# Kernel optimization log

Measured on AMD Instinct MI355X. Metric: run time of the kernel, lower is better.

## Reference

```python
import jax, jax.numpy as jnp
import numpy as np

N, E = 100000, 640000
IN_DIM, OUT_DIM, MSG_DIM, TIME_DIM, HEADS = 128, 128, 128, 128, 2
C = OUT_DIM // HEADS  # per-head channels = 64
EDGE_DIM = MSG_DIM + TIME_DIM  # 256


def setup_inputs() -> dict:
    key = jax.random.key(0)
    ks = jax.random.split(key, 16)
    s = 0.05
    return {
        "x": jax.random.normal(ks[0], (N, IN_DIM), jnp.float32),
        "last_update": jax.random.uniform(ks[1], (N,), jnp.float32, 0.0, 100.0),
        "t": jax.random.uniform(ks[2], (E,), jnp.float32, 100.0, 200.0),
        "msg": jax.random.normal(ks[3], (E, MSG_DIM), jnp.float32),
        "time_w": jax.random.normal(ks[4], (TIME_DIM,), jnp.float32) * s,
        "time_b": jax.random.normal(ks[5], (TIME_DIM,), jnp.float32) * s,
        "Wq": jax.random.normal(ks[6], (IN_DIM, HEADS * C), jnp.float32) * s,
        "bq": jnp.zeros((HEADS * C,), jnp.float32),
        "Wk": jax.random.normal(ks[7], (IN_DIM, HEADS * C), jnp.float32) * s,
        "bk": jnp.zeros((HEADS * C,), jnp.float32),
        "Wv": jax.random.normal(ks[8], (IN_DIM, HEADS * C), jnp.float32) * s,
        "bv": jnp.zeros((HEADS * C,), jnp.float32),
        "We": jax.random.normal(ks[9], (EDGE_DIM, HEADS * C), jnp.float32) * s,
        "Wskip": jax.random.normal(ks[10], (IN_DIM, HEADS * C), jnp.float32) * s,
        "bskip": jnp.zeros((HEADS * C,), jnp.float32),
        "edge_index": jax.random.randint(ks[11], (2, E), 0, N, jnp.int64),
    }


def reference(x, last_update, t, msg, time_w, time_b, Wq, bq, Wk, bk, Wv, bv,
              We, Wskip, bskip, edge_index):
    src = edge_index[0]  # source node j per edge
    dst = edge_index[1]  # target node i per edge

    # Time encoding: phi(dt) = cos(w*dt + b)
    rel_t = t - last_update[src]                      # [E]
    rel_t_enc = jnp.cos(rel_t[:, None] * time_w[None, :] + time_b)  # [E, TIME_DIM]
    edge_attr = jnp.concatenate([rel_t_enc, msg], axis=-1)           # [E, EDGE_DIM]

    # Node-level projections (dense GEMMs), then edge gathers
    q_n = x @ Wq + bq   # [N, H*C]
    k_n = x @ Wk + bk
    v_n = x @ Wv + bv
    e_proj = (edge_attr @ We).reshape(E, HEADS, C)    # [E, H, C]

    q = q_n[dst].reshape(E, HEADS, C)
    k = k_n[src].reshape(E, HEADS, C) + e_proj
    v = v_n[src].reshape(E, HEADS, C) + e_proj

    # Per-edge attention logits, scatter-softmax over incoming edges of each dst
    alpha = jnp.sum(q * k, axis=-1) / jnp.sqrt(jnp.float32(C))  # [E, H]
    a_max = jax.ops.segment_max(alpha, dst, num_segments=N)      # [N, H]
    a_max = jnp.where(jnp.isfinite(a_max), a_max, 0.0)
    a_exp = jnp.exp(alpha - a_max[dst])                          # [E, H]
    a_sum = jax.ops.segment_sum(a_exp, dst, num_segments=N)      # [N, H]
    attn = a_exp / (a_sum[dst] + 1e-16)                          # [E, H]

    # Weighted aggregate + skip connection (concat heads)
    out = jax.ops.segment_sum(attn[..., None] * v, dst, num_segments=N)  # [N, H, C]
    out = out.reshape(N, HEADS * C) + (x @ Wskip + bskip)
    return out
```

## Files before the change

kernel.cpp:

```cpp
#include <hip/hip_runtime.h>
#include <hip/hip_bf16.h>

#define NN 100000
#define EE 640000
#define NB_SCAN 98
#define G_E3 2048

typedef short bf16x8 __attribute__((ext_vector_type(8)));
typedef float f32x4 __attribute__((ext_vector_type(4)));

__device__ __forceinline__ ushort f2bf(float f){
  uint u = __float_as_uint(f);
  u += 0x7fffu + ((u >> 16) & 1u);
  return (ushort)(u >> 16);
}
__device__ __forceinline__ float bf2f(ushort s){ return __uint_as_float(((uint)s) << 16); }
__device__ __forceinline__ uint pack2(float a, float b){ return ((uint)f2bf(b) << 16) | (uint)f2bf(a); }
__device__ __forceinline__ uint swz(uint row, uint colB, uint strideB){
  return row * strideB + (colB ^ ((row & 7u) << 4));
}

__global__ void k_prep(const float* __restrict__ Wq, const float* __restrict__ Wk,
                       const float* __restrict__ Wv, const float* __restrict__ Wsk,
                       const float* __restrict__ We,
                       ushort* __restrict__ W4t, ushort* __restrict__ Wet,
                       int* __restrict__ deg){
  int tid = blockIdx.x * 256 + threadIdx.x;
  if (tid < 512 * 128){
    int col = tid >> 7, k = tid & 127;
    const float* W = (col < 128) ? Wq : ((col < 256) ? Wk : ((col < 384) ? Wv : Wsk));
    W4t[tid] = f2bf(W[k * 128 + (col & 127)]);
  }
  if (tid < 128 * 256){
    int col = tid >> 8, k = tid & 255;
    Wet[tid] = f2bf(We[k * 128 + col]);
  }
  if (tid < NN) deg[tid] = 0;
}

__global__ __launch_bounds__(256) void k_node(
    const float* __restrict__ x, const ushort* __restrict__ W4t,
    const float* __restrict__ bq, const float* __restrict__ bk,
    const float* __restrict__ bv, const float* __restrict__ bsk,
    ushort* __restrict__ q_n, ushort* __restrict__ kv,
    float* __restrict__ out){
  __shared__ ushort As[64 * 128];
  __shared__ ushort Bs[128 * 128];
  char* Ab = (char*)As; char* Bb = (char*)Bs;
  int tid = threadIdx.x;
  int n0 = blockIdx.x * 64;
  {
    int row = tid >> 2, part = tid & 3;
    int gr = n0 + row;
    for (int j = 0; j < 4; j++){
      float4 a = make_float4(0.f,0.f,0.f,0.f), b = a;
      if (gr < NN){
        const float4* p = (const float4*)(x + (size_t)gr * 128 + part * 32 + j * 8);
        a = p[0]; b = p[1];
      }
      uint4 w; w.x = pack2(a.x,a.y); w.y = pack2(a.z,a.w); w.z = pack2(b.x,b.y); w.w = pack2(b.z,b.w);
      *(uint4*)(Ab + swz(row, (uint)(part * 64 + j * 16), 256)) = w;
    }
  }
  int wid = tid >> 6, l = tid & 63, lr = l & 15, lg = l >> 4;
  for (int chunk = 0; chunk < 4; ++chunk){
    if (chunk) __syncthreads();
    {
      int row = tid >> 1, half = tid & 1;
      const ushort* src = W4t + (size_t)(chunk * 128 + row) * 128 + half * 64;
      for (int j = 0; j < 8; j++){
        uint4 w = *(const uint4*)(src + j * 8);
        *(uint4*)(Bb + swz(row, (uint)(half * 128 + j * 16), 256)) = w;
      }
    }
    __syncthreads();
    f32x4 acc[8];
    for (int i = 0; i < 8; i++) acc[i] = (f32x4){0.f,0.f,0.f,0.f};
    for (int ks = 0; ks < 4; ++ks){
      bf16x8 a = *(bf16x8*)(Ab + swz(wid * 16 + lr, (uint)(ks * 64 + lg * 16), 256));
      for (int cf = 0; cf < 8; ++cf){
        bf16x8 b = *(bf16x8*)(Bb + swz(cf * 16 + lr, (uint)(ks * 64 + lg * 16), 256));
        acc[cf] = __builtin_amdgcn_mfma_f32_16x16x32_bf16(a, b, acc[cf], 0, 0, 0);
      }
    }
    for (int cf = 0; cf < 8; ++cf){
      for (int i = 0; i < 4; i++){
        int row = wid * 16 + lg * 4 + i;
        int gr = n0 + row;
        if (gr >= NN) continue;
        int col = cf * 16 + lr;
        float v = acc[cf][i];
        if (chunk == 0)      q_n[(size_t)gr * 128 + col] = f2bf(v + bq[col]);
        else if (chunk == 1) kv[(size_t)gr * 256 + ((col >> 1) << 2) + (col & 1)]     = f2bf(v + bk[col]);
        else if (chunk == 2) kv[(size_t)gr * 256 + ((col >> 1) << 2) + 2 + (col & 1)] = f2bf(v + bv[col]);
        else                 out[(size_t)gr * 128 + col] = v + bsk[col];
      }
    }
  }
}

__global__ void k_rel(const float* __restrict__ tt, const float* __restrict__ lu,
                      const int* __restrict__ ei, float* __restrict__ rel){
  int e = blockIdx.x * 256 + threadIdx.x;
  if (e < EE) rel[e] = tt[e] - lu[ei[e]];
}

__global__ __launch_bounds__(256, 2) void k_edge3(
    const float* __restrict__ rel, const float* __restrict__ msg,
    const float* __restrict__ tw, const float* __restrict__ tb,
    const ushort* __restrict__ Wet, ushort* __restrict__ ep){
  int tid = threadIdx.x;
  int wid = tid >> 6, l = tid & 63, lr = l & 15, lg = l >> 4;
  int gw = (int)blockIdx.x * 4 + wid;
  int half = gw & 1;
  bf16x8 Af[4][8];
  const char* WB = (const char*)Wet;
  #pragma unroll
  for (int rt = 0; rt < 4; ++rt)
    #pragma unroll
    for (int ks = 0; ks < 8; ++ks)
      Af[rt][ks] = *(const bf16x8*)(WB + (size_t)(half*64 + rt*16 + lr)*512 + ks*64 + lg*16);

  for (int g = gw >> 1; g < EE/16; g += G_E3 * 2){
    int e0 = g * 16;
    float4 m[8];
    const float* MB = msg + (size_t)(e0 + lr) * 128 + lg * 8;
    #pragma unroll
    for (int ks = 0; ks < 4; ++ks){
      m[2*ks]   = *(const float4*)(MB + ks * 32);
      m[2*ks+1] = *(const float4*)(MB + ks * 32 + 4);
    }
    float relv = rel[e0 + lr];
    bf16x8 B[8];
    #pragma unroll
    for (int ks = 0; ks < 4; ++ks){
      int k0 = ks * 32 + lg * 8;
      float4 wa = *(const float4*)(tw + k0), wb = *(const float4*)(tw + k0 + 4);
      float4 ba = *(const float4*)(tb + k0), bb = *(const float4*)(tb + k0 + 4);
      float c0 = __cosf(fmaf(relv, wa.x, ba.x));
      float c1 = __cosf(fmaf(relv, wa.y, ba.y));
      float c2 = __cosf(fmaf(relv, wa.z, ba.z));
      float c3 = __cosf(fmaf(relv, wa.w, ba.w));
      float c4 = __cosf(fmaf(relv, wb.x, bb.x));
      float c5 = __cosf(fmaf(relv, wb.y, bb.y));
      float c6 = __cosf(fmaf(relv, wb.z, bb.z));
      float c7 = __cosf(fmaf(relv, wb.w, bb.w));
      uint4 w; w.x = pack2(c0,c1); w.y = pack2(c2,c3); w.z = pack2(c4,c5); w.w = pack2(c6,c7);
      B[ks] = *(bf16x8*)&w;
    }
    #pragma unroll
    for (int ks = 0; ks < 4; ++ks){
      float4 a = m[2*ks], b = m[2*ks+1];
      uint4 w; w.x = pack2(a.x,a.y); w.y = pack2(a.z,a.w); w.z = pack2(b.x,b.y); w.w = pack2(b.z,b.w);
      B[4+ks] = *(bf16x8*)&w;
    }
    f32x4 acc[4];
    #pragma unroll
    for (int rt = 0; rt < 4; ++rt) acc[rt] = (f32x4){0.f,0.f,0.f,0.f};
    #pragma unroll
    for (int ks = 0; ks < 8; ++ks)
      #pragma unroll
      for (int rt = 0; rt < 4; ++rt)
        acc[rt] = __builtin_amdgcn_mfma_f32_16x16x32_bf16(Af[rt][ks], B[ks], acc[rt], 0, 0, 0);
    #pragma unroll
    for (int rt = 0; rt < 4; ++rt){
      uint2 w = make_uint2(pack2(acc[rt][0], acc[rt][1]), pack2(acc[rt][2], acc[rt][3]));
      *(uint2*)(ep + (size_t)(e0 + lr) * 128 + half * 64 + rt * 16 + lg * 4) = w;
    }
  }
}

__global__ void k_hist(const int* __restrict__ ei, int* __restrict__ deg){
  int e = blockIdx.x * 256 + threadIdx.x;
  if (e < EE) atomicAdd(&deg[ei[EE + e]], 1);
}

__global__ __launch_bounds__(256) void k_scan1(const int* __restrict__ deg,
                                               int* __restrict__ start,
                                               int* __restrict__ partial){
  __shared__ int sums[256];
  int b = blockIdx.x, tid = threadIdx.x;
  int base = b * 1024 + tid * 4;
  int d0 = (base + 0 < NN) ? deg[base + 0] : 0;
  int d1 = (base + 1 < NN) ? deg[base + 1] : 0;
  int d2 = (base + 2 < NN) ? deg[base + 2] : 0;
  int d3 = (base + 3 < NN) ? deg[base + 3] : 0;
  int s = d0 + d1 + d2 + d3;
  sums[tid] = s;
  __syncthreads();
  for (int off = 1; off < 256; off <<= 1){
    int v = (tid >= off) ? sums[tid - off] : 0;
    __syncthreads();
    sums[tid] += v;
    __syncthreads();
  }
  int excl = sums[tid] - s;
  if (base + 0 < NN) start[base + 0] = excl;
  if (base + 1 < NN) start[base + 1] = excl + d0;
  if (base + 2 < NN) start[base + 2] = excl + d0 + d1;
  if (base + 3 < NN) start[base + 3] = excl + d0 + d1 + d2;
  if (tid == 255) partial[b] = sums[255];
}

__global__ void k_scan2(int* __restrict__ partial){
  if (threadIdx.x == 0){
    int run = 0;
    for (int b = 0; b < NB_SCAN; b++){ int t = partial[b]; partial[b] = run; run += t; }
  }
}

__global__ void k_scan3(int* __restrict__ start, const int* __restrict__ partial,
                        int* __restrict__ cursor){
  int i = blockIdx.x * 256 + threadIdx.x;
  if (i < NN){
    int v = start[i] + partial[i >> 10];
    start[i] = v;
    cursor[i] = v;
  }
  if (i == 0) start[NN] = EE;
}

__global__ void k_place(const int* __restrict__ ei, int* __restrict__ cursor,
                        uint2* __restrict__ sorted2){
  int e = blockIdx.x * 256 + threadIdx.x;
  if (e < EE){
    int dst = ei[EE + e];
    int src = ei[e];
    int pos = atomicAdd(&cursor[dst], 1);
    sorted2[pos] = make_uint2((uint)e, (uint)src);
  }
}

__global__ __launch_bounds__(256) void k_gather(
    const ushort* __restrict__ q_n, const ushort* __restrict__ kv,
    const ushort* __restrict__ ep, const int* __restrict__ start,
    const uint2* __restrict__ sorted2, float* __restrict__ out){
  int wave = (blockIdx.x * 256 + threadIdx.x) >> 6;
  if (wave >= NN) return;
  int n = wave;
  int l = threadIdx.x & 63;
  int c = l * 2;
  int s0 = start[n], s1 = start[n + 1];
  uint qq = *(const uint*)(q_n + (size_t)n * 128 + c);
  float q0 = bf2f(qq & 0xffff), q1 = bf2f(qq >> 16);
  float acc0 = 0.f, acc1 = 0.f, denom = 0.f;
  int i = s0;
  for (; i + 2 <= s1; i += 2){
    uint2 p0 = sorted2[i], p1 = sorted2[i + 1];
    uint2 kv0 = *(const uint2*)(kv + (size_t)p0.y * 256 + c * 2);
    uint2 kv1 = *(const uint2*)(kv + (size_t)p1.y * 256 + c * 2);
    uint e0 = *(const uint*)(ep + (size_t)p0.x * 128 + c);
    uint e1 = *(const uint*)(ep + (size_t)p1.x * 128 + c);
    float pa0 = bf2f(e0 & 0xffff), pa1 = bf2f(e0 >> 16);
    float pb0 = bf2f(e1 & 0xffff), pb1 = bf2f(e1 >> 16);
    float ka = q0 * (bf2f(kv0.x & 0xffff) + pa0) + q1 * (bf2f(kv0.x >> 16) + pa1);
    float kb = q0 * (bf2f(kv1.x & 0xffff) + pb0) + q1 * (bf2f(kv1.x >> 16) + pb1);
    #pragma unroll
    for (int off = 16; off > 0; off >>= 1){
      ka += __shfl_xor(ka, off);
      kb += __shfl_xor(kb, off);
    }
    float ea = __expf(ka * 0.125f), eb = __expf(kb * 0.125f);
    denom += ea + eb;
    acc0 += ea * (bf2f(kv0.y & 0xffff) + pa0) + eb * (bf2f(kv1.y & 0xffff) + pb0);
    acc1 += ea * (bf2f(kv0.y >> 16) + pa1) + eb * (bf2f(kv1.y >> 16) + pb1);
  }
  if (i < s1){
    uint2 p0 = sorted2[i];
    uint2 kv0 = *(const uint2*)(kv + (size_t)p0.y * 256 + c * 2);
    uint e0 = *(const uint*)(ep + (size_t)p0.x * 128 + c);
    float pa0 = bf2f(e0 & 0xffff), pa1 = bf2f(e0 >> 16);
    float ka = q0 * (bf2f(kv0.x & 0xffff) + pa0) + q1 * (bf2f(kv0.x >> 16) + pa1);
    #pragma unroll
    for (int off = 16; off > 0; off >>= 1) ka += __shfl_xor(ka, off);
    float ea = __expf(ka * 0.125f);
    denom += ea;
    acc0 += ea * (bf2f(kv0.y & 0xffff) + pa0);
    acc1 += ea * (bf2f(kv0.y >> 16) + pa1);
  }
  float inv = 1.0f / (denom + 1e-16f);
  size_t o = (size_t)n * 128 + c;
  out[o]     += acc0 * inv;
  out[o + 1] += acc1 * inv;
}

extern "C" void kernel_launch(void* const* d_in, const int* in_sizes, int n_in,
                              void* d_out, int out_size, void* d_ws, size_t ws_size,
                              hipStream_t stream) {
  const float* x   = (const float*)d_in[0];
  const float* lu  = (const float*)d_in[1];
  const float* t   = (const float*)d_in[2];
  const float* msg = (const float*)d_in[3];
  const float* tw  = (const float*)d_in[4];
  const float* tb  = (const float*)d_in[5];
  const float* Wq  = (const float*)d_in[6];
  const float* bq  = (const float*)d_in[7];
  const float* Wk  = (const float*)d_in[8];
  const float* bk  = (const float*)d_in[9];
  const float* Wv  = (const float*)d_in[10];
  const float* bv  = (const float*)d_in[11];
  const float* We  = (const float*)d_in[12];
  const float* Wsk = (const float*)d_in[13];
  const float* bsk = (const float*)d_in[14];
  const int*   ei  = (const int*)d_in[15];
  float* out = (float*)d_out;

  char* w = (char*)d_ws;
  size_t off = 0;
  auto nxt = [&](size_t b){ size_t r = off; off += (b + 255) & ~(size_t)255; return r; };
  ushort* q_n   = (ushort*)(w + nxt((size_t)NN * 128 * 2));
  ushort* kv    = (ushort*)(w + nxt((size_t)NN * 256 * 2));
  ushort* epj   = (ushort*)(w + nxt((size_t)EE * 128 * 2));
  ushort* W4t   = (ushort*)(w + nxt((size_t)512 * 128 * 2));
  ushort* Wet   = (ushort*)(w + nxt((size_t)128 * 256 * 2));
  int* deg      = (int*)(w + nxt((size_t)NN * 4));
  int* start    = (int*)(w + nxt((size_t)(NN + 1) * 4));
  int* cursor   = (int*)(w + nxt((size_t)NN * 4));
  int* partial  = (int*)(w + nxt((size_t)(NB_SCAN + 1) * 4));
  uint2* sorted2 = (uint2*)(w + nxt((size_t)EE * 8));
  float* rel    = (float*)(w + nxt((size_t)EE * 4));

  k_prep<<<(NN + 255) / 256, 256, 0, stream>>>(Wq, Wk, Wv, Wsk, We, W4t, Wet, deg);
  k_node<<<(NN + 63) / 64, 256, 0, stream>>>(x, W4t, bq, bk, bv, bsk, q_n, kv, out);
  k_rel<<<(EE + 255) / 256, 256, 0, stream>>>(t, lu, ei, rel);
  k_edge3<<<G_E3, 256, 0, stream>>>(rel, msg, tw, tb, Wet, epj);
  k_hist<<<(EE + 255) / 256, 256, 0, stream>>>(ei, deg);
  k_scan1<<<NB_SCAN, 256, 0, stream>>>(deg, start, partial);
  k_scan2<<<1, 64, 0, stream>>>(partial);
  k_scan3<<<(NN + 255) / 256, 256, 0, stream>>>(start, partial, cursor);
  k_place<<<(EE + 255) / 256, 256, 0, stream>>>(ei, cursor, sorted2);
  k_gather<<<(NN * 64 + 255) / 256, 256, 0, stream>>>(q_n, kv, epj, start, sorted2, out);
}
```

Before: 479.7 us.

## Compute edge projections in dst-sorted order so gather reads them contiguously

Edge sorting now runs before the edge projection kernel. k_place also computes the relative time per sorted position, and the separate k_rel kernel is removed. The new k_edge4 reads msg rows through the sorted edge index (a random gather) and writes the projections in sorted order, so k_gather reads them contiguously instead of by random edge id. Each wave now covers 32 of the 128 output columns rather than 64, with more blocks and higher occupancy, and the next tile's index and time are prefetched. The cost is that msg reads become scattered, and the sort now sits on the critical path before the edge GEMM.

Result: slower. 602.5 us (+25.6%).

```diff
diff --git a/kernel.cpp b/kernel.cpp
--- a/kernel.cpp
+++ b/kernel.cpp
@@ -4,7 +4,7 @@
 #define NN 100000
 #define EE 640000
 #define NB_SCAN 98
-#define G_E3 2048
+#define G_E4 4096
 
 typedef short bf16x8 __attribute__((ext_vector_type(8)));
 typedef float f32x4 __attribute__((ext_vector_type(4)));
@@ -99,77 +99,6 @@
   }
 }
 
-__global__ void k_rel(const float* __restrict__ tt, const float* __restrict__ lu,
-                      const int* __restrict__ ei, float* __restrict__ rel){
-  int e = blockIdx.x * 256 + threadIdx.x;
-  if (e < EE) rel[e] = tt[e] - lu[ei[e]];
-}
-
-__global__ __launch_bounds__(256, 2) void k_edge3(
-    const float* __restrict__ rel, const float* __restrict__ msg,
-    const float* __restrict__ tw, const float* __restrict__ tb,
-    const ushort* __restrict__ Wet, ushort* __restrict__ ep){
-  int tid = threadIdx.x;
-  int wid = tid >> 6, l = tid & 63, lr = l & 15, lg = l >> 4;
-  int gw = (int)blockIdx.x * 4 + wid;
-  int half = gw & 1;
-  bf16x8 Af[4][8];
-  const char* WB = (const char*)Wet;
-  #pragma unroll
-  for (int rt = 0; rt < 4; ++rt)
-    #pragma unroll
-    for (int ks = 0; ks < 8; ++ks)
-      Af[rt][ks] = *(const bf16x8*)(WB + (size_t)(half*64 + rt*16 + lr)*512 + ks*64 + lg*16);
-
-  for (int g = gw >> 1; g < EE/16; g += G_E3 * 2){
-    int e0 = g * 16;
-    float4 m[8];
-    const float* MB = msg + (size_t)(e0 + lr) * 128 + lg * 8;
-    #pragma unroll
-    for (int ks = 0; ks < 4; ++ks){
-      m[2*ks]   = *(const float4*)(MB + ks * 32);
-      m[2*ks+1] = *(const float4*)(MB + ks * 32 + 4);
-    }
-    float relv = rel[e0 + lr];
-    bf16x8 B[8];
-    #pragma unroll
-    for (int ks = 0; ks < 4; ++ks){
-      int k0 = ks * 32 + lg * 8;
-      float4 wa = *(const float4*)(tw + k0), wb = *(const float4*)(tw + k0 + 4);
-      float4 ba = *(const float4*)(tb + k0), bb = *(const float4*)(tb + k0 + 4);
-      float c0 = __cosf(fmaf(relv, wa.x, ba.x));
-      float c1 = __cosf(fmaf(relv, wa.y, ba.y));
-      float c2 = __cosf(fmaf(relv, wa.z, ba.z));
-      float c3 = __cosf(fmaf(relv, wa.w, ba.w));
-      float c4 = __cosf(fmaf(relv, wb.x, bb.x));
-      float c5 = __cosf(fmaf(relv, wb.y, bb.y));
-      float c6 = __cosf(fmaf(relv, wb.z, bb.z));
-      float c7 = __cosf(fmaf(relv, wb.w, bb.w));
-      uint4 w; w.x = pack2(c0,c1); w.y = pack2(c2,c3); w.z = pack2(c4,c5); w.w = pack2(c6,c7);
-      B[ks] = *(bf16x8*)&w;
-    }
-    #pragma unroll
-    for (int ks = 0; ks < 4; ++ks){
-      float4 a = m[2*ks], b = m[2*ks+1];
-      uint4 w; w.x = pack2(a.x,a.y); w.y = pack2(a.z,a.w); w.z = pack2(b.x,b.y); w.w = pack2(b.z,b.w);
-      B[4+ks] = *(bf16x8*)&w;
-    }
-    f32x4 acc[4];
-    #pragma unroll
-    for (int rt = 0; rt < 4; ++rt) acc[rt] = (f32x4){0.f,0.f,0.f,0.f};
-    #pragma unroll
-    for (int ks = 0; ks < 8; ++ks)
-      #pragma unroll
-      for (int rt = 0; rt < 4; ++rt)
-        acc[rt] = __builtin_amdgcn_mfma_f32_16x16x32_bf16(Af[rt][ks], B[ks], acc[rt], 0, 0, 0);
-    #pragma unroll
-    for (int rt = 0; rt < 4; ++rt){
-      uint2 w = make_uint2(pack2(acc[rt][0], acc[rt][1]), pack2(acc[rt][2], acc[rt][3]));
-      *(uint2*)(ep + (size_t)(e0 + lr) * 128 + half * 64 + rt * 16 + lg * 4) = w;
-    }
-  }
-}
-
 __global__ void k_hist(const int* __restrict__ ei, int* __restrict__ deg){
   int e = blockIdx.x * 256 + threadIdx.x;
   if (e < EE) atomicAdd(&deg[ei[EE + e]], 1);
@@ -220,21 +149,96 @@
   if (i == 0) start[NN] = EE;
 }
 
-__global__ void k_place(const int* __restrict__ ei, int* __restrict__ cursor,
-                        uint2* __restrict__ sorted2){
+__global__ void k_place(const int* __restrict__ ei, const float* __restrict__ tt,
+                        const float* __restrict__ lu, int* __restrict__ cursor,
+                        uint* __restrict__ srcs, uint* __restrict__ eidx,
+                        float* __restrict__ rel_s){
   int e = blockIdx.x * 256 + threadIdx.x;
   if (e < EE){
     int dst = ei[EE + e];
     int src = ei[e];
     int pos = atomicAdd(&cursor[dst], 1);
-    sorted2[pos] = make_uint2((uint)e, (uint)src);
+    srcs[pos] = (uint)src;
+    eidx[pos] = (uint)e;
+    rel_s[pos] = tt[e] - lu[src];
+  }
+}
+
+__global__ __launch_bounds__(256, 3) void k_edge4(
+    const float* __restrict__ rel_s, const float* __restrict__ msg,
+    const float* __restrict__ tw, const float* __restrict__ tb,
+    const uint* __restrict__ eidx, const ushort* __restrict__ Wet,
+    ushort* __restrict__ ep_s){
+  int tid = threadIdx.x;
+  int wid = tid >> 6, l = tid & 63, lr = l & 15, lg = l >> 4;
+  bf16x8 Af[2][8];
+  const char* WB = (const char*)Wet;
+  #pragma unroll
+  for (int rt = 0; rt < 2; ++rt)
+    #pragma unroll
+    for (int ks = 0; ks < 8; ++ks)
+      Af[rt][ks] = *(const bf16x8*)(WB + (size_t)(wid*32 + rt*16 + lr)*512 + ks*64 + lg*16);
+
+  int tile = blockIdx.x;
+  uint eN = 0; float relN = 0.f;
+  if (tile < EE/16){ eN = eidx[tile*16 + lr]; relN = rel_s[tile*16 + lr]; }
+  for (; tile < EE/16; tile += G_E4){
+    int p0 = tile * 16;
+    uint e = eN; float relv = relN;
+    const float* MB = msg + (size_t)e * 128 + lg * 8;
+    float4 m[8];
+    #pragma unroll
+    for (int ks = 0; ks < 4; ++ks){
+      m[2*ks]   = *(const float4*)(MB + ks * 32);
+      m[2*ks+1] = *(const float4*)(MB + ks * 32 + 4);
+    }
+    if (tile + G_E4 < EE/16){
+      eN = eidx[(tile + G_E4)*16 + lr];
+      relN = rel_s[(tile + G_E4)*16 + lr];
+    }
+    bf16x8 B[8];
+    #pragma unroll
+    for (int ks = 0; ks < 4; ++ks){
+      int k0 = ks * 32 + lg * 8;
+      float4 wa = *(const float4*)(tw + k0), wb = *(const float4*)(tw + k0 + 4);
+      float4 ba = *(const float4*)(tb + k0), bb = *(const float4*)(tb + k0 + 4);
+      float c0 = __cosf(fmaf(relv, wa.x, ba.x));
+      float c1 = __cosf(fmaf(relv, wa.y, ba.y));
+      float c2 = __cosf(fmaf(relv, wa.z, ba.z));
+      float c3 = __cosf(fmaf(relv, wa.w, ba.w));
+      float c4 = __cosf(fmaf(relv, wb.x, bb.x));
+      float c5 = __cosf(fmaf(relv, wb.y, bb.y));
+      float c6 = __cosf(fmaf(relv, wb.z, bb.z));
+      float c7 = __cosf(fmaf(relv, wb.w, bb.w));
+      uint4 w; w.x = pack2(c0,c1); w.y = pack2(c2,c3); w.z = pack2(c4,c5); w.w = pack2(c6,c7);
+      B[ks] = *(bf16x8*)&w;
+    }
+    #pragma unroll
+    for (int ks = 0; ks < 4; ++ks){
+      float4 a = m[2*ks], b = m[2*ks+1];
+      uint4 w; w.x = pack2(a.x,a.y); w.y = pack2(a.z,a.w); w.z = pack2(b.x,b.y); w.w = pack2(b.z,b.w);
+      B[4+ks] = *(bf16x8*)&w;
+    }
+    f32x4 acc[2];
+    #pragma unroll
+    for (int rt = 0; rt < 2; ++rt) acc[rt] = (f32x4){0.f,0.f,0.f,0.f};
+    #pragma unroll
+    for (int ks = 0; ks < 8; ++ks)
+      #pragma unroll
+      for (int rt = 0; rt < 2; ++rt)
+        acc[rt] = __builtin_amdgcn_mfma_f32_16x16x32_bf16(Af[rt][ks], B[ks], acc[rt], 0, 0, 0);
+    #pragma unroll
+    for (int rt = 0; rt < 2; ++rt){
+      uint2 w = make_uint2(pack2(acc[rt][0], acc[rt][1]), pack2(acc[rt][2], acc[rt][3]));
+      *(uint2*)(ep_s + (size_t)(p0 + lr) * 128 + wid * 32 + rt * 16 + lg * 4) = w;
+    }
   }
 }
 
 __global__ __launch_bounds__(256) void k_gather(
     const ushort* __restrict__ q_n, const ushort* __restrict__ kv,
-    const ushort* __restrict__ ep, const int* __restrict__ start,
-    const uint2* __restrict__ sorted2, float* __restrict__ out){
+    const ushort* __restrict__ ep_s, const int* __restrict__ start,
+    const uint* __restrict__ srcs, float* __restrict__ out){
   int wave = (blockIdx.x * 256 + threadIdx.x) >> 6;
   if (wave >= NN) return;
   int n = wave;
@@ -246,11 +250,11 @@
   float acc0 = 0.f, acc1 = 0.f, denom = 0.f;
   int i = s0;
   for (; i + 2 <= s1; i += 2){
-    uint2 p0 = sorted2[i], p1 = sorted2[i + 1];
-    uint2 kv0 = *(const uint2*)(kv + (size_t)p0.y * 256 + c * 2);
-    uint2 kv1 = *(const uint2*)(kv + (size_t)p1.y * 256 + c * 2);
-    uint e0 = *(const uint*)(ep + (size_t)p0.x * 128 + c);
-    uint e1 = *(const uint*)(ep + (size_t)p1.x * 128 + c);
+    uint sa = srcs[i], sb = srcs[i + 1];
+    uint2 kv0 = *(const uint2*)(kv + (size_t)sa * 256 + c * 2);
+    uint2 kv1 = *(const uint2*)(kv + (size_t)sb * 256 + c * 2);
+    uint e0 = *(const uint*)(ep_s + (size_t)i * 128 + c);
+    uint e1 = *(const uint*)(ep_s + (size_t)(i + 1) * 128 + c);
     float pa0 = bf2f(e0 & 0xffff), pa1 = bf2f(e0 >> 16);
     float pb0 = bf2f(e1 & 0xffff), pb1 = bf2f(e1 >> 16);
     float ka = q0 * (bf2f(kv0.x & 0xffff) + pa0) + q1 * (bf2f(kv0.x >> 16) + pa1);
@@ -266,9 +270,9 @@
     acc1 += ea * (bf2f(kv0.y >> 16) + pa1) + eb * (bf2f(kv1.y >> 16) + pb1);
   }
   if (i < s1){
-    uint2 p0 = sorted2[i];
-    uint2 kv0 = *(const uint2*)(kv + (size_t)p0.y * 256 + c * 2);
-    uint e0 = *(const uint*)(ep + (size_t)p0.x * 128 + c);
+    uint sa = srcs[i];
+    uint2 kv0 = *(const uint2*)(kv + (size_t)sa * 256 + c * 2);
+    uint e0 = *(const uint*)(ep_s + (size_t)i * 128 + c);
     float pa0 = bf2f(e0 & 0xffff), pa1 = bf2f(e0 >> 16);
     float ka = q0 * (bf2f(kv0.x & 0xffff) + pa0) + q1 * (bf2f(kv0.x >> 16) + pa1);
     #pragma unroll
@@ -310,24 +314,24 @@
   auto nxt = [&](size_t b){ size_t r = off; off += (b + 255) & ~(size_t)255; return r; };
   ushort* q_n   = (ushort*)(w + nxt((size_t)NN * 128 * 2));
   ushort* kv    = (ushort*)(w + nxt((size_t)NN * 256 * 2));
-  ushort* epj   = (ushort*)(w + nxt((size_t)EE * 128 * 2));
+  ushort* ep_s  = (ushort*)(w + nxt((size_t)EE * 128 * 2));
   ushort* W4t   = (ushort*)(w + nxt((size_t)512 * 128 * 2));
   ushort* Wet   = (ushort*)(w + nxt((size_t)128 * 256 * 2));
   int* deg      = (int*)(w + nxt((size_t)NN * 4));
   int* start    = (int*)(w + nxt((size_t)(NN + 1) * 4));
   int* cursor   = (int*)(w + nxt((size_t)NN * 4));
   int* partial  = (int*)(w + nxt((size_t)(NB_SCAN + 1) * 4));
-  uint2* sorted2 = (uint2*)(w + nxt((size_t)EE * 8));
-  float* rel    = (float*)(w + nxt((size_t)EE * 4));
+  uint* srcs    = (uint*)(w + nxt((size_t)EE * 4));
+  uint* eidx    = (uint*)(w + nxt((size_t)EE * 4));
+  float* rel_s  = (float*)(w + nxt((size_t)EE * 4));
 
   k_prep<<<(NN + 255) / 256, 256, 0, stream>>>(Wq, Wk, Wv, Wsk, We, W4t, Wet, deg);
   k_node<<<(NN + 63) / 64, 256, 0, stream>>>(x, W4t, bq, bk, bv, bsk, q_n, kv, out);
-  k_rel<<<(EE + 255) / 256, 256, 0, stream>>>(t, lu, ei, rel);
-  k_edge3<<<G_E3, 256, 0, stream>>>(rel, msg, tw, tb, Wet, epj);
   k_hist<<<(EE + 255) / 256, 256, 0, stream>>>(ei, deg);
   k_scan1<<<NB_SCAN, 256, 0, stream>>>(deg, start, partial);
   k_scan2<<<1, 64, 0, stream>>>(partial);
   k_scan3<<<(NN + 255) / 256, 256, 0, stream>>>(start, partial, cursor);
-  k_place<<<(EE + 255) / 256, 256, 0, stream>>>(ei, cursor, sorted2);
-  k_gather<<<(NN * 64 + 255) / 256, 256, 0, stream>>>(q_n, kv, epj, start, sorted2, out);
-}
+  k_place<<<(EE + 255) / 256, 256, 0, stream>>>(ei, t, lu, cursor, srcs, eidx, rel_s);
+  k_edge4<<<G_E4, 256, 0, stream>>>(rel_s, msg, tw, tb, eidx, Wet, ep_s);
+  k_gather<<<(NN * 64 + 255) / 256, 256, 0, stream>>>(q_n, kv, ep_s, start, srcs, out);
+}
```

## Split edge projection output across four waves per tile and unroll gather by four

Applied to the files above, without the earlier changes.

The edge-projection kernel now assigns each block one 16-edge tile, with its four waves each computing a 32-column quarter. Previously each wave computed 64 columns of a tile. This halves the weight fragments held in registers, allows four blocks per CU and launches more blocks, which should raise occupancy and memory-level parallelism. The trade-off is that each wave now redoes the cosine time encoding and the msg loads for its tile, so that work is duplicated four ways. Separately, the gather kernel gains a 4-edge unrolled loop so that more independent kv and ep loads are in flight per wave.

Result: slower. 843.8 us (+75.9%).

```diff
diff --git a/kernel.cpp b/kernel.cpp
--- a/kernel.cpp
+++ b/kernel.cpp
@@ -4,7 +4,7 @@
 #define NN 100000
 #define EE 640000
 #define NB_SCAN 98
-#define G_E3 2048
+#define G_E5 8192
 
 typedef short bf16x8 __attribute__((ext_vector_type(8)));
 typedef float f32x4 __attribute__((ext_vector_type(4)));
@@ -105,26 +105,25 @@
   if (e < EE) rel[e] = tt[e] - lu[ei[e]];
 }
 
-__global__ __launch_bounds__(256, 2) void k_edge3(
+__global__ __launch_bounds__(256, 4) void k_edge5(
     const float* __restrict__ rel, const float* __restrict__ msg,
     const float* __restrict__ tw, const float* __restrict__ tb,
     const ushort* __restrict__ Wet, ushort* __restrict__ ep){
   int tid = threadIdx.x;
   int wid = tid >> 6, l = tid & 63, lr = l & 15, lg = l >> 4;
-  int gw = (int)blockIdx.x * 4 + wid;
-  int half = gw & 1;
-  bf16x8 Af[4][8];
+  int quar = wid;
+  bf16x8 Af[2][8];
   const char* WB = (const char*)Wet;
   #pragma unroll
-  for (int rt = 0; rt < 4; ++rt)
+  for (int rt = 0; rt < 2; ++rt)
     #pragma unroll
     for (int ks = 0; ks < 8; ++ks)
-      Af[rt][ks] = *(const bf16x8*)(WB + (size_t)(half*64 + rt*16 + lr)*512 + ks*64 + lg*16);
-
-  for (int g = gw >> 1; g < EE/16; g += G_E3 * 2){
-    int e0 = g * 16;
+      Af[rt][ks] = *(const bf16x8*)(WB + (size_t)(quar*32 + rt*16 + lr)*512 + ks*64 + lg*16);
+
+  for (int tile = blockIdx.x; tile < EE/16; tile += G_E5){
+    int e0 = tile * 16;
+    const float* MB = msg + (size_t)(e0 + lr) * 128 + lg * 8;
     float4 m[8];
-    const float* MB = msg + (size_t)(e0 + lr) * 128 + lg * 8;
     #pragma unroll
     for (int ks = 0; ks < 4; ++ks){
       m[2*ks]   = *(const float4*)(MB + ks * 32);
@@ -154,18 +153,18 @@
       uint4 w; w.x = pack2(a.x,a.y); w.y = pack2(a.z,a.w); w.z = pack2(b.x,b.y); w.w = pack2(b.z,b.w);
       B[4+ks] = *(bf16x8*)&w;
     }
-    f32x4 acc[4];
-    #pragma unroll
-    for (int rt = 0; rt < 4; ++rt) acc[rt] = (f32x4){0.f,0.f,0.f,0.f};
+    f32x4 acc[2];
+    #pragma unroll
+    for (int rt = 0; rt < 2; ++rt) acc[rt] = (f32x4){0.f,0.f,0.f,0.f};
     #pragma unroll
     for (int ks = 0; ks < 8; ++ks)
       #pragma unroll
-      for (int rt = 0; rt < 4; ++rt)
+      for (int rt = 0; rt < 2; ++rt)
         acc[rt] = __builtin_amdgcn_mfma_f32_16x16x32_bf16(Af[rt][ks], B[ks], acc[rt], 0, 0, 0);
     #pragma unroll
-    for (int rt = 0; rt < 4; ++rt){
+    for (int rt = 0; rt < 2; ++rt){
       uint2 w = make_uint2(pack2(acc[rt][0], acc[rt][1]), pack2(acc[rt][2], acc[rt][3]));
-      *(uint2*)(ep + (size_t)(e0 + lr) * 128 + half * 64 + rt * 16 + lg * 4) = w;
+      *(uint2*)(ep + (size_t)(e0 + lr) * 128 + quar * 32 + rt * 16 + lg * 4) = w;
     }
   }
 }
@@ -245,6 +244,39 @@
   float q0 = bf2f(qq & 0xffff), q1 = bf2f(qq >> 16);
   float acc0 = 0.f, acc1 = 0.f, denom = 0.f;
   int i = s0;
+  for (; i + 4 <= s1; i += 4){
+    uint2 p0 = sorted2[i], p1 = sorted2[i+1], p2 = sorted2[i+2], p3 = sorted2[i+3];
+    uint2 kv0 = *(const uint2*)(kv + (size_t)p0.y * 256 + c * 2);
+    uint2 kv1 = *(const uint2*)(kv + (size_t)p1.y * 256 + c * 2);
+    uint2 kv2 = *(const uint2*)(kv + (size_t)p2.y * 256 + c * 2);
+    uint2 kv3 = *(const uint2*)(kv + (size_t)p3.y * 256 + c * 2);
+    uint e0 = *(const uint*)(ep + (size_t)p0.x * 128 + c);
+    uint e1 = *(const uint*)(ep + (size_t)p1.x * 128 + c);
+    uint e2 = *(const uint*)(ep + (size_t)p2.x * 128 + c);
+    uint e3 = *(const uint*)(ep + (size_t)p3.x * 128 + c);
+    float pa0 = bf2f(e0 & 0xffff), pa1 = bf2f(e0 >> 16);
+    float pb0 = bf2f(e1 & 0xffff), pb1 = bf2f(e1 >> 16);
+    float pc0 = bf2f(e2 & 0xffff), pc1 = bf2f(e2 >> 16);
+    float pd0 = bf2f(e3 & 0xffff), pd1 = bf2f(e3 >> 16);
+    float ka = q0 * (bf2f(kv0.x & 0xffff) + pa0) + q1 * (bf2f(kv0.x >> 16) + pa1);
+    float kb = q0 * (bf2f(kv1.x & 0xffff) + pb0) + q1 * (bf2f(kv1.x >> 16) + pb1);
+    float kc = q0 * (bf2f(kv2.x & 0xffff) + pc0) + q1 * (bf2f(kv2.x >> 16) + pc1);
+    float kd = q0 * (bf2f(kv3.x & 0xffff) + pd0) + q1 * (bf2f(kv3.x >> 16) + pd1);
+    #pragma unroll
+    for (int off = 16; off > 0; off >>= 1){
+      ka += __shfl_xor(ka, off);
+      kb += __shfl_xor(kb, off);
+      kc += __shfl_xor(kc, off);
+      kd += __shfl_xor(kd, off);
+    }
+    float ea = __expf(ka * 0.125f), eb = __expf(kb * 0.125f);
+    float ec = __expf(kc * 0.125f), ed = __expf(kd * 0.125f);
+    denom += (ea + eb) + (ec + ed);
+    acc0 += ea * (bf2f(kv0.y & 0xffff) + pa0) + eb * (bf2f(kv1.y & 0xffff) + pb0)
+          + ec * (bf2f(kv2.y & 0xffff) + pc0) + ed * (bf2f(kv3.y & 0xffff) + pd0);
+    acc1 += ea * (bf2f(kv0.y >> 16) + pa1) + eb * (bf2f(kv1.y >> 16) + pb1)
+          + ec * (bf2f(kv2.y >> 16) + pc1) + ed * (bf2f(kv3.y >> 16) + pd1);
+  }
   for (; i + 2 <= s1; i += 2){
     uint2 p0 = sorted2[i], p1 = sorted2[i + 1];
     uint2 kv0 = *(const uint2*)(kv + (size_t)p0.y * 256 + c * 2);
@@ -323,7 +355,7 @@
   k_prep<<<(NN + 255) / 256, 256, 0, stream>>>(Wq, Wk, Wv, Wsk, We, W4t, Wet, deg);
   k_node<<<(NN + 63) / 64, 256, 0, stream>>>(x, W4t, bq, bk, bv, bsk, q_n, kv, out);
   k_rel<<<(EE + 255) / 256, 256, 0, stream>>>(t, lu, ei, rel);
-  k_edge3<<<G_E3, 256, 0, stream>>>(rel, msg, tw, tb, Wet, epj);
+  k_edge5<<<G_E5, 256, 0, stream>>>(rel, msg, tw, tb, Wet, epj);
   k_hist<<<(EE + 255) / 256, 256, 0, stream>>>(ei, deg);
   k_scan1<<<NB_SCAN, 256, 0, stream>>>(deg, start, partial);
   k_scan2<<<1, 64, 0, stream>>>(partial);
```
